# Optimization experiments

Measured on AMD Instinct MI355X. Metric: run time of the kernel, lower is better.

Reference implementation:

```python
import jax, jax.numpy as jnp
import numpy as np

B, S, D_MODEL, N_HEADS = 4, 2048, 1024, 16
HEAD_DIM = D_MODEL // N_HEADS  # 64; used only for the softmax scale, as in the source


def setup_inputs() -> dict:
    key = jax.random.key(0)
    kq, kk, kv, kw = jax.random.split(key, 4)
    q = jax.random.normal(kq, (B, S, D_MODEL), dtype=jnp.float32)
    k = jax.random.normal(kk, (B, S, D_MODEL), dtype=jnp.float32)
    v = jax.random.normal(kv, (B, S, D_MODEL), dtype=jnp.float32)
    # out_proj: nn.Linear(d_model, d_model, bias=False) -> weight [out, in]
    W_out = jax.random.normal(kw, (D_MODEL, D_MODEL), dtype=jnp.float32) * (1.0 / np.sqrt(D_MODEL))
    return {"q": q, "k": k, "v": v, "W_out": W_out}


def reference(q, k, v, W_out):
    scale = 1.0 / jnp.sqrt(jnp.float32(HEAD_DIM))
    # scores: [B, Sq, Sk] -- full quadratic score matrix, as in the source
    scores = jnp.einsum("bqd,bkd->bqk", q, k) * scale
    attn = jax.nn.softmax(scores, axis=-1)
    out = jnp.einsum("bqk,bkd->bqd", attn, v)
    # torch Linear: y = x @ W^T
    return jnp.einsum("bsd,ed->bse", out, W_out)
```

## Files before the change

kernel.cpp:

```cpp
#include <hip/hip_runtime.h>
#include <hip/hip_fp16.h>
#include <stdint.h>

typedef _Float16 h16;
typedef _Float16 h16x8 __attribute__((ext_vector_type(8)));
typedef float f32x4 __attribute__((ext_vector_type(4)));

#define BB 4
#define SS 2048
#define DD 1024

__device__ __forceinline__ void gload16(const void* g, void* l) {
    __builtin_amdgcn_global_load_lds(
        (const __attribute__((address_space(1))) uint32_t*)g,
        (__attribute__((address_space(3))) uint32_t*)l, 16, 0, 0);
}

__global__ __launch_bounds__(256) void cvt_f32_h16(const float* __restrict__ in,
                                                   h16* __restrict__ out,
                                                   int n8, float scale) {
    int i = blockIdx.x * 256 + threadIdx.x;
    if (i >= n8) return;
    const float4* p = (const float4*)in + (size_t)i * 2;
    float4 a = p[0], b = p[1];
    union { int4 i4; h16 h[8]; } u;
    u.h[0] = (h16)(a.x * scale); u.h[1] = (h16)(a.y * scale);
    u.h[2] = (h16)(a.z * scale); u.h[3] = (h16)(a.w * scale);
    u.h[4] = (h16)(b.x * scale); u.h[5] = (h16)(b.y * scale);
    u.h[6] = (h16)(b.z * scale); u.h[7] = (h16)(b.w * scale);
    ((int4*)out)[i] = u.i4;
}

#define SLOTS_A 1024
#define SLOTS_T 3072

template<bool F32OUT>
__global__ __launch_bounds__(512, 2) void gemm_bt(
    const h16* __restrict__ A, const h16* __restrict__ B, void* __restrict__ Cv,
    int lda, int ldb, int ldc, int K, int tilesN, int tilesMN,
    long long aBatch, long long bBatch, long long cBatch)
{
    __shared__ h16 lds[3 * SLOTS_T * 8];

    const int tid = threadIdx.x;
    const int nwg = gridDim.x;
    const int bid = blockIdx.x;
    const int wgid = (bid & 7) * (nwg >> 3) + (bid >> 3);
    const int bb  = wgid / tilesMN;
    const int rem = wgid % tilesMN;
    const int tm = rem / tilesN, tn = rem % tilesN;
    const int row0 = tm * 128, col0 = tn * 256;

    const h16* Ab = A + (long long)bb * aBatch;
    const h16* Bb = B + (long long)bb * bBatch;

    const int lane = tid & 63, wid = tid >> 6;
    const int wm = wid >> 2, wn = wid & 3;
    const int frow = lane & 15;
    const int kq = lane >> 4;
    const int xr = frow & 7;

    const int sg = (((tid & 7) ^ ((tid >> 3) & 7)) * 8);
    const int sr = tid >> 3;

    const int NT = K >> 6;

    f32x4 acc[4][4];
#pragma unroll
    for (int m = 0; m < 4; ++m)
#pragma unroll
        for (int n = 0; n < 4; ++n) acc[m][n] = (f32x4){0.f, 0.f, 0.f, 0.f};

    auto STAGE = [&](int kt, int buf) {
        const h16* as = Ab + (size_t)(row0 + sr) * lda + kt + sg;
        const h16* bs = Bb + (size_t)(col0 + sr) * ldb + kt + sg;
        h16* la = lds + ((size_t)buf * SLOTS_T + tid) * 8;
        h16* lb = lds + ((size_t)buf * SLOTS_T + SLOTS_A + tid) * 8;
#pragma unroll
        for (int i = 0; i < 2; ++i)
            gload16(as + (size_t)i * 64 * lda, la + (size_t)i * 512 * 8);
#pragma unroll
        for (int i = 0; i < 4; ++i)
            gload16(bs + (size_t)i * 64 * ldb, lb + (size_t)i * 512 * 8);
    };

    STAGE(0, 0);
    STAGE(64, 1);
    asm volatile("s_waitcnt vmcnt(6)" ::: "memory");
    __builtin_amdgcn_s_barrier();
    __builtin_amdgcn_sched_barrier(0);

    int cur = 0;
    for (int t = 0; t < NT; ++t) {
        if (t + 2 < NT) STAGE((t + 2) << 6, (cur == 0) ? 2 : cur - 1);
        const h16* bufp = lds + (size_t)cur * (SLOTS_T * 8);
#pragma unroll
        for (int ks = 0; ks < 2; ++ks) {
            const int g8 = (((kq + 4 * ks) ^ xr) * 8);
            h16x8 af[4], bf[4];
#pragma unroll
            for (int m = 0; m < 4; ++m)
                af[m] = *(const h16x8*)(bufp + (wm * 64 + m * 16 + frow) * 64 + g8);
#pragma unroll
            for (int n = 0; n < 4; ++n)
                bf[n] = *(const h16x8*)(bufp + SLOTS_A * 8 + (wn * 64 + n * 16 + frow) * 64 + g8);
            __builtin_amdgcn_s_setprio(1);
#pragma unroll
            for (int m = 0; m < 4; ++m)
#pragma unroll
                for (int n = 0; n < 4; ++n)
                    acc[m][n] = __builtin_amdgcn_mfma_f32_16x16x32_f16(af[m], bf[n], acc[m][n], 0, 0, 0);
            __builtin_amdgcn_s_setprio(0);
        }
        if (t == NT - 1) break;
        if (t + 2 < NT) asm volatile("s_waitcnt vmcnt(6) lgkmcnt(0)" ::: "memory");
        else            asm volatile("s_waitcnt vmcnt(0) lgkmcnt(0)" ::: "memory");
        __builtin_amdgcn_s_barrier();
        __builtin_amdgcn_sched_barrier(0);
        cur = (cur == 2) ? 0 : cur + 1;
    }

    const int erow = row0 + wm * 64 + (lane >> 4) * 4;
    const int ecol = col0 + wn * 64 + (lane & 15);
    if (F32OUT) {
        float* C = (float*)Cv + (long long)bb * cBatch;
#pragma unroll
        for (int m = 0; m < 4; ++m)
#pragma unroll
            for (int n = 0; n < 4; ++n)
#pragma unroll
                for (int j = 0; j < 4; ++j)
                    C[(size_t)(erow + m * 16 + j) * ldc + (ecol + n * 16)] = acc[m][n][j];
    } else {
        h16* C = (h16*)Cv + (long long)bb * cBatch;
#pragma unroll
        for (int m = 0; m < 4; ++m)
#pragma unroll
            for (int n = 0; n < 4; ++n)
#pragma unroll
                for (int j = 0; j < 4; ++j)
                    C[(size_t)(erow + m * 16 + j) * ldc + (ecol + n * 16)] = (h16)acc[m][n][j];
    }
}

__global__ __launch_bounds__(256) void softmax_rows(h16* __restrict__ buf) {
    const int row = blockIdx.x;
    h16* rp = buf + (size_t)row * 2048;
    const int t = threadIdx.x;
    const int lane = t & 63, wid = t >> 6;

    union { int4 i4; h16 h[8]; } u;
    u.i4 = ((const int4*)rp)[t];
    float f[8];
#pragma unroll
    for (int j = 0; j < 8; ++j) f[j] = (float)u.h[j];

    float m = f[0];
#pragma unroll
    for (int j = 1; j < 8; ++j) m = fmaxf(m, f[j]);
#pragma unroll
    for (int off = 32; off; off >>= 1) m = fmaxf(m, __shfl_xor(m, off));

    __shared__ float smax[4];
    __shared__ float ssum[4];
    if (lane == 0) smax[wid] = m;
    __syncthreads();
    m = fmaxf(fmaxf(smax[0], smax[1]), fmaxf(smax[2], smax[3]));

    float s = 0.f;
#pragma unroll
    for (int j = 0; j < 8; ++j) { f[j] = __expf(f[j] - m); s += f[j]; }
#pragma unroll
    for (int off = 32; off; off >>= 1) s += __shfl_xor(s, off);
    if (lane == 0) ssum[wid] = s;
    __syncthreads();
    float inv = 1.0f / (ssum[0] + ssum[1] + ssum[2] + ssum[3]);

#pragma unroll
    for (int j = 0; j < 8; ++j) u.h[j] = (h16)(f[j] * inv);
    ((int4*)rp)[t] = u.i4;
}

extern "C" void kernel_launch(void* const* d_in, const int* in_sizes, int n_in,
                              void* d_out, int out_size, void* d_ws, size_t ws_size,
                              hipStream_t stream) {
    (void)in_sizes; (void)n_in; (void)out_size; (void)ws_size;
    const float* q = (const float*)d_in[0];
    const float* k = (const float*)d_in[1];
    const float* v = (const float*)d_in[2];
    const float* w = (const float*)d_in[3];
    float* out = (float*)d_out;

    const size_t QKV = (size_t)BB * SS * DD;
    h16* qh = (h16*)d_ws;
    h16* kh = qh + QKV;
    h16* vh = kh + QKV;
    h16* wh = vh + QKV;
    h16* sc = wh + (size_t)DD * DD;

    cvt_f32_h16<<<(int)(QKV / 8 + 255) / 256, 256, 0, stream>>>(q, qh, (int)(QKV / 8), 0.125f);
    cvt_f32_h16<<<(int)(QKV / 8 + 255) / 256, 256, 0, stream>>>(k, kh, (int)(QKV / 8), 1.0f);
    cvt_f32_h16<<<(int)(QKV / 8 + 255) / 256, 256, 0, stream>>>(v, vh, (int)(QKV / 8), 1.0f);
    cvt_f32_h16<<<(DD * DD / 8 + 255) / 256, 256, 0, stream>>>(w, wh, DD * DD / 8, 1.0f);

    gemm_bt<false><<<512, 512, 0, stream>>>(
        qh, kh, (void*)sc, DD, DD, SS, DD, 8, 128,
        (long long)SS * DD, (long long)SS * DD, (long long)SS * SS);

    softmax_rows<<<BB * SS, 256, 0, stream>>>(sc);

    h16* vpT = qh;
    gemm_bt<false><<<256, 512, 0, stream>>>(
        wh, vh, (void*)vpT, DD, DD, BB * SS, DD, 32, 256,
        0LL, 0LL, 0LL);

    gemm_bt<true><<<256, 512, 0, stream>>>(
        sc, vpT, (void*)out, SS, BB * SS, DD, SS, 4, 64,
        (long long)SS * SS, (long long)SS, (long long)SS * DD);
}
```

Baseline: 156.4 us.

## Replace GEMM with double-buffered quadrant-interleaved pipeline and 256-row tiles for QK^T

The GEMM kernel is rewritten as a double-buffered, 8-phase schedule. Each K-step is split into four MFMA quadrants, and the global-to-LDS loads for later stages are interleaved between them with explicit barriers and wait counts. The intent is to overlap memory traffic with matrix-core work at finer granularity. The QK^T GEMM now uses 256x256 tiles, which halves the grid to 256 workgroups and gives more operand reuse. The trade-off is many more barriers per iteration, only two LDS buffers instead of three, and higher register pressure for the BM=256 variant.

```diff
diff --git a/kernel.cpp b/kernel.cpp
--- a/kernel.cpp
+++ b/kernel.cpp
@@ -31,16 +31,22 @@
     ((int4*)out)[i] = u.i4;
 }
 
-#define SLOTS_A 1024
-#define SLOTS_T 3072
-
-template<bool F32OUT>
-__global__ __launch_bounds__(512, 2) void gemm_bt(
+template<int BM, bool F32OUT>
+__global__ __launch_bounds__(512, 2) void gemm8p(
     const h16* __restrict__ A, const h16* __restrict__ B, void* __restrict__ Cv,
     int lda, int ldb, int ldc, int K, int tilesN, int tilesMN,
     long long aBatch, long long bBatch, long long cBatch)
 {
-    __shared__ h16 lds[3 * SLOTS_T * 8];
+    constexpr int WROWS  = BM / 2;
+    constexpr int MF     = WROWS / 16;
+    constexpr int MQ     = MF / 2;
+    constexpr int AH     = WROWS / 2;
+    constexpr int ALOADS = BM / 128;
+    constexpr int ABYTES = BM * 128;
+    constexpr int BBYTES = 256 * 128;
+    constexpr int BUFB   = ABYTES + BBYTES;
+
+    __shared__ __align__(1024) char lds[2 * BUFB];
 
     const int tid = threadIdx.x;
     const int nwg = gridDim.x;
@@ -49,83 +55,139 @@
     const int bb  = wgid / tilesMN;
     const int rem = wgid % tilesMN;
     const int tm = rem / tilesN, tn = rem % tilesN;
-    const int row0 = tm * 128, col0 = tn * 256;
+    const int row0 = tm * BM, col0 = tn * 256;
 
     const h16* Ab = A + (long long)bb * aBatch;
     const h16* Bb = B + (long long)bb * bBatch;
 
     const int lane = tid & 63, wid = tid >> 6;
     const int wm = wid >> 2, wn = wid & 3;
-    const int frow = lane & 15;
-    const int kq = lane >> 4;
-    const int xr = frow & 7;
-
-    const int sg = (((tid & 7) ^ ((tid >> 3) & 7)) * 8);
-    const int sr = tid >> 3;
+    const int frow = lane & 15, kq = lane >> 4;
 
     const int NT = K >> 6;
 
-    f32x4 acc[4][4];
-#pragma unroll
-    for (int m = 0; m < 4; ++m)
+    f32x4 acc[MF][4];
+#pragma unroll
+    for (int m = 0; m < MF; ++m)
 #pragma unroll
         for (int n = 0; n < 4; ++n) acc[m][n] = (f32x4){0.f, 0.f, 0.f, 0.f};
 
-    auto STAGE = [&](int kt, int buf) {
-        const h16* as = Ab + (size_t)(row0 + sr) * lda + kt + sg;
-        const h16* bs = Bb + (size_t)(col0 + sr) * ldb + kt + sg;
-        h16* la = lds + ((size_t)buf * SLOTS_T + tid) * 8;
-        h16* lb = lds + ((size_t)buf * SLOTS_T + SLOTS_A + tid) * 8;
-#pragma unroll
-        for (int i = 0; i < 2; ++i)
-            gload16(as + (size_t)i * 64 * lda, la + (size_t)i * 512 * 8);
-#pragma unroll
-        for (int i = 0; i < 4; ++i)
-            gload16(bs + (size_t)i * 64 * ldb, lb + (size_t)i * 512 * 8);
-    };
-
-    STAGE(0, 0);
-    STAGE(64, 1);
-    asm volatile("s_waitcnt vmcnt(6)" ::: "memory");
+    char* l0 = (char*)lds;
+
+    auto STAGE_A = [&](int kt, int buf, int mh) {
+#pragma unroll
+        for (int i = 0; i < ALOADS; ++i) {
+            int d = wid * (ALOADS * 64) + i * 64 + lane;
+            int s = d & 7, hr = d >> 3;
+            int r = ((hr & ~(AH - 1)) << 1) + mh * AH + (hr & (AH - 1));
+            int gg = s ^ (r & 7);
+            gload16(Ab + (size_t)(row0 + r) * lda + kt + gg * 8,
+                    l0 + buf * BUFB + (r * 8 + s) * 16);
+        }
+    };
+    auto STAGE_B = [&](int kt, int buf, int nh) {
+#pragma unroll
+        for (int i = 0; i < 2; ++i) {
+            int d = wid * 128 + i * 64 + lane;
+            int s = d & 7, hr = d >> 3;
+            int r = ((hr & ~31) << 1) + nh * 32 + (hr & 31);
+            int gg = s ^ (r & 7);
+            gload16(Bb + (size_t)(col0 + r) * ldb + kt + gg * 8,
+                    l0 + buf * BUFB + ABYTES + (r * 8 + s) * 16);
+        }
+    };
+    auto READ_A = [&](int buf, int mh, h16x8 (&af)[MQ][2]) {
+#pragma unroll
+        for (int mm = 0; mm < MQ; ++mm)
+#pragma unroll
+            for (int ks = 0; ks < 2; ++ks) {
+                int r = wm * WROWS + (mh * MQ + mm) * 16 + frow;
+                int s = (ks * 4 + kq) ^ (r & 7);
+                af[mm][ks] = *(const h16x8*)(l0 + buf * BUFB + (r * 8 + s) * 16);
+            }
+    };
+    auto READ_B = [&](int buf, int nh, h16x8 (&bf)[2][2]) {
+#pragma unroll
+        for (int nn = 0; nn < 2; ++nn)
+#pragma unroll
+            for (int ks = 0; ks < 2; ++ks) {
+                int r = wn * 64 + (nh * 2 + nn) * 16 + frow;
+                int s = (ks * 4 + kq) ^ (r & 7);
+                bf[nn][ks] = *(const h16x8*)(l0 + buf * BUFB + ABYTES + (r * 8 + s) * 16);
+            }
+    };
+    auto MFMA_Q = [&](int mh, int nh, h16x8 (&af)[MQ][2], h16x8 (&bf)[2][2]) {
+        __builtin_amdgcn_s_setprio(1);
+#pragma unroll
+        for (int mm = 0; mm < MQ; ++mm)
+#pragma unroll
+            for (int nn = 0; nn < 2; ++nn)
+#pragma unroll
+                for (int ks = 0; ks < 2; ++ks)
+                    acc[mh * MQ + mm][nh * 2 + nn] =
+                        __builtin_amdgcn_mfma_f32_16x16x32_f16(
+                            af[mm][ks], bf[nn][ks], acc[mh * MQ + mm][nh * 2 + nn], 0, 0, 0);
+        __builtin_amdgcn_s_setprio(0);
+    };
+    auto WAIT_LGKM_PIN = [&]() {
+        asm volatile("s_waitcnt lgkmcnt(0)" ::: "memory");
+        __builtin_amdgcn_sched_barrier(0);
+    };
+
+    STAGE_A(0, 0, 0); STAGE_B(0, 0, 0); STAGE_B(0, 0, 1); STAGE_A(0, 0, 1);
+    STAGE_A(64, 1, 0); STAGE_B(64, 1, 0); STAGE_B(64, 1, 1);
+    if constexpr (BM == 256) asm volatile("s_waitcnt vmcnt(6)" ::: "memory");
+    else                     asm volatile("s_waitcnt vmcnt(5)" ::: "memory");
     __builtin_amdgcn_s_barrier();
-    __builtin_amdgcn_sched_barrier(0);
-
-    int cur = 0;
-    for (int t = 0; t < NT; ++t) {
-        if (t + 2 < NT) STAGE((t + 2) << 6, (cur == 0) ? 2 : cur - 1);
-        const h16* bufp = lds + (size_t)cur * (SLOTS_T * 8);
-#pragma unroll
-        for (int ks = 0; ks < 2; ++ks) {
-            const int g8 = (((kq + 4 * ks) ^ xr) * 8);
-            h16x8 af[4], bf[4];
-#pragma unroll
-            for (int m = 0; m < 4; ++m)
-                af[m] = *(const h16x8*)(bufp + (wm * 64 + m * 16 + frow) * 64 + g8);
-#pragma unroll
-            for (int n = 0; n < 4; ++n)
-                bf[n] = *(const h16x8*)(bufp + SLOTS_A * 8 + (wn * 64 + n * 16 + frow) * 64 + g8);
-            __builtin_amdgcn_s_setprio(1);
-#pragma unroll
-            for (int m = 0; m < 4; ++m)
-#pragma unroll
-                for (int n = 0; n < 4; ++n)
-                    acc[m][n] = __builtin_amdgcn_mfma_f32_16x16x32_f16(af[m], bf[n], acc[m][n], 0, 0, 0);
-            __builtin_amdgcn_s_setprio(0);
+
+    h16x8 af[MQ][2], bf0[2][2], bf1[2][2];
+
+    for (int G = 0; G < NT; ++G) {
+        const int buf = G & 1;
+        const int kt1 = (G + 1) << 6, kt2 = (G + 2) << 6;
+        READ_A(buf, 0, af);
+        READ_B(buf, 0, bf0);
+        if (G + 1 < NT) STAGE_A(kt1, buf ^ 1, 1);
+        __builtin_amdgcn_s_barrier();
+        WAIT_LGKM_PIN();
+        MFMA_Q(0, 0, af, bf0);
+        __builtin_amdgcn_sched_barrier(0);
+        __builtin_amdgcn_s_barrier();
+        READ_B(buf, 1, bf1);
+        if (G + 2 < NT) STAGE_A(kt2, buf, 0);
+        __builtin_amdgcn_s_barrier();
+        WAIT_LGKM_PIN();
+        MFMA_Q(0, 1, af, bf1);
+        __builtin_amdgcn_sched_barrier(0);
+        __builtin_amdgcn_s_barrier();
+        READ_A(buf, 1, af);
+        if (G + 2 < NT) STAGE_B(kt2, buf, 0);
+        __builtin_amdgcn_s_barrier();
+        WAIT_LGKM_PIN();
+        MFMA_Q(1, 0, af, bf0);
+        __builtin_amdgcn_sched_barrier(0);
+        __builtin_amdgcn_s_barrier();
+        if (G + 2 < NT) STAGE_B(kt2, buf, 1);
+        __builtin_amdgcn_s_barrier();
+        WAIT_LGKM_PIN();
+        MFMA_Q(1, 1, af, bf1);
+        __builtin_amdgcn_sched_barrier(0);
+        if (G + 2 >= NT) {
+            asm volatile("s_waitcnt vmcnt(0)" ::: "memory");
+        } else if constexpr (BM == 256) {
+            asm volatile("s_waitcnt vmcnt(6)" ::: "memory");
+        } else {
+            asm volatile("s_waitcnt vmcnt(5)" ::: "memory");
         }
-        if (t == NT - 1) break;
-        if (t + 2 < NT) asm volatile("s_waitcnt vmcnt(6) lgkmcnt(0)" ::: "memory");
-        else            asm volatile("s_waitcnt vmcnt(0) lgkmcnt(0)" ::: "memory");
-        __builtin_amdgcn_s_barrier();
-        __builtin_amdgcn_sched_barrier(0);
-        cur = (cur == 2) ? 0 : cur + 1;
+        __builtin_amdgcn_s_barrier();
     }
 
-    const int erow = row0 + wm * 64 + (lane >> 4) * 4;
+    const int erow = row0 + wm * WROWS + (lane >> 4) * 4;
     const int ecol = col0 + wn * 64 + (lane & 15);
     if (F32OUT) {
         float* C = (float*)Cv + (long long)bb * cBatch;
 #pragma unroll
-        for (int m = 0; m < 4; ++m)
+        for (int m = 0; m < MF; ++m)
 #pragma unroll
             for (int n = 0; n < 4; ++n)
 #pragma unroll
@@ -134,7 +196,7 @@
     } else {
         h16* C = (h16*)Cv + (long long)bb * cBatch;
 #pragma unroll
-        for (int m = 0; m < 4; ++m)
+        for (int m = 0; m < MF; ++m)
 #pragma unroll
             for (int n = 0; n < 4; ++n)
 #pragma unroll
@@ -203,18 +265,18 @@
     cvt_f32_h16<<<(int)(QKV / 8 + 255) / 256, 256, 0, stream>>>(v, vh, (int)(QKV / 8), 1.0f);
     cvt_f32_h16<<<(DD * DD / 8 + 255) / 256, 256, 0, stream>>>(w, wh, DD * DD / 8, 1.0f);
 
-    gemm_bt<false><<<512, 512, 0, stream>>>(
-        qh, kh, (void*)sc, DD, DD, SS, DD, 8, 128,
+    gemm8p<256, false><<<256, 512, 0, stream>>>(
+        qh, kh, (void*)sc, DD, DD, SS, DD, 8, 64,
         (long long)SS * DD, (long long)SS * DD, (long long)SS * SS);
 
     softmax_rows<<<BB * SS, 256, 0, stream>>>(sc);
 
     h16* vpT = qh;
-    gemm_bt<false><<<256, 512, 0, stream>>>(
+    gemm8p<128, false><<<256, 512, 0, stream>>>(
         wh, vh, (void*)vpT, DD, DD, BB * SS, DD, 32, 256,
         0LL, 0LL, 0LL);
 
-    gemm_bt<true><<<256, 512, 0, stream>>>(
+    gemm8p<128, true><<<256, 512, 0, stream>>>(
         sc, vpT, (void*)out, SS, BB * SS, DD, SS, 4, 64,
         (long long)SS * SS, (long long)SS, (long long)SS * DD);
 }
```

After: 150.9 us. -3.5%, faster.
